# Kernel optimization log

Measured on AMD Instinct MI355X. Metric: run time of the kernel, lower is better.

## Reference

```python
import jax, jax.numpy as jnp
import numpy as np

B, S, D, H, DFF = 8, 1024, 1024, 16, 4096
DK = D // H
NEG = -1000000000.0


def layernorm(x, g, b, eps=1e-5):
    mu = jnp.mean(x, axis=-1, keepdims=True)
    var = jnp.mean((x - mu) ** 2, axis=-1, keepdims=True)
    return (x - mu) / jnp.sqrt(var + eps) * g + b


def setup_inputs() -> dict:
    key = jax.random.key(0)
    ks = jax.random.split(key, 16)
    s = 0.02
    inp = {
        "x": jax.random.normal(ks[0], (B, S, D), jnp.float32),
        "binary_mask": jax.random.randint(ks[1], (B, S), 0, 2, jnp.int32),
        # per-head projections stacked: [H, D, DK]
        "Wq": jax.random.normal(ks[2], (H, D, DK), jnp.float32) * s,
        "bq": jnp.zeros((H, DK), jnp.float32),
        "Wk": jax.random.normal(ks[3], (H, D, DK), jnp.float32) * s,
        "bk": jnp.zeros((H, DK), jnp.float32),
        "Wv": jax.random.normal(ks[4], (H, D, DK), jnp.float32) * s,
        "bv": jnp.zeros((H, DK), jnp.float32),
        "Wo": jax.random.normal(ks[5], (D, D), jnp.float32) * s,
        "bo": jnp.zeros((D,), jnp.float32),
        "ga": jnp.ones((D,), jnp.float32),
        "ba": jnp.zeros((D,), jnp.float32),
        "W1": jax.random.normal(ks[6], (D, DFF), jnp.float32) * s,
        "b1": jnp.zeros((DFF,), jnp.float32),
        "W2": jax.random.normal(ks[7], (DFF, D), jnp.float32) * s,
        "b2": jnp.zeros((D,), jnp.float32),
        "gf": jnp.ones((D,), jnp.float32),
        "bf": jnp.zeros((D,), jnp.float32),
    }
    return inp


def encoder_fwd(x, binary_mask, Wq, bq, Wk, bk, Wv, bv, Wo, bo, ga, ba, W1, b1, W2, b2, gf, bf):
    # --- multi-head self-attention (heads vectorized over h axis) ---
    q = jnp.einsum("bsd,hdk->bhsk", x, Wq) + bq[None, :, None, :]
    k = jnp.einsum("bsd,hdk->bhsk", x, Wk) + bk[None, :, None, :]
    v = jnp.einsum("bsd,hdk->bhsk", x, Wv) + bv[None, :, None, :]
    score = jnp.einsum("bhik,bhjk->bhij", q, k) / jnp.sqrt(jnp.float32(DK))
    # mask: binary_mask is over KEY positions, broadcast over query dim
    score = score + jnp.where(binary_mask[:, None, None, :] == 0, NEG, 0.0)
    # NOTE: original code softmaxes over dim=1 of [B,Sq,Sk] -> the QUERY axis
    probs = jax.nn.softmax(score, axis=2)
    ctx = jnp.einsum("bhij,bhjk->bhik", probs, v)  # [B,H,S,DK]
    ctx = jnp.transpose(ctx, (0, 2, 1, 3)).reshape(x.shape[0], x.shape[1], D)
    attn_out = ctx @ Wo + bo
    y = layernorm(x + attn_out, ga, ba)
    # --- FFN ---
    h = jax.nn.relu(y @ W1 + b1)
    ffn_out = h @ W2 + b2
    return layernorm(y + ffn_out, gf, bf)


def reference(x, binary_mask, Wq, bq, Wk, bk, Wv, bv, Wo, bo, ga, ba, W1, b1, W2, b2, gf, bf):
    return encoder_fwd(x, binary_mask, Wq, bq, Wk, bk, Wv, bv, Wo, bo, ga, ba, W1, b1, W2, b2, gf, bf)
```

## Files before the change

kernel.cpp:

```cpp
#include <hip/hip_runtime.h>
#include <hip/hip_bf16.h>

typedef __bf16 bf16;
typedef __bf16 bf16x8 __attribute__((ext_vector_type(8)));
typedef __bf16 bf16x4 __attribute__((ext_vector_type(4)));
typedef float  f32x4  __attribute__((ext_vector_type(4)));

#define NB 8
#define NS 1024
#define ND 1024
#define NH 16
#define NDK 64
#define NDFF 4096

static __device__ __forceinline__ f32x4 mfma16(bf16x8 a, bf16x8 b, f32x4 c) {
    return __builtin_amdgcn_mfma_f32_16x16x32_bf16(a, b, c, 0, 0, 0);
}

#define GLDS(g, l) __builtin_amdgcn_global_load_lds( \
    (const __attribute__((address_space(1))) void*)(g), \
    (__attribute__((address_space(3))) void*)(l), 16, 0, 0)

__global__ __launch_bounds__(256) void prep_all(
    const float* __restrict__ x, const int* __restrict__ mask,
    const float* __restrict__ Wq, const float* __restrict__ Wk, const float* __restrict__ Wv,
    const float* __restrict__ Wo, const float* __restrict__ W1, const float* __restrict__ W2,
    const float* __restrict__ bq, const float* __restrict__ bk, const float* __restrict__ bv,
    bf16* __restrict__ xb, bf16* __restrict__ wqkvT, bf16* __restrict__ WoT,
    bf16* __restrict__ W1T, bf16* __restrict__ W2T, float* __restrict__ bqkv,
    int* __restrict__ newpos, int* __restrict__ Ucnt, float* __restrict__ cvec)
{
    __shared__ __align__(16) char shraw[64 * 65 * 4];
    int bid = blockIdx.x, t = threadIdx.x;
    if (bid < 8192) {
        int idx = bid * 256 + t;
        float4 v = ((const float4*)x)[idx];
        bf16x4 o = { (bf16)v.x, (bf16)v.y, (bf16)v.z, (bf16)v.w };
        ((bf16x4*)xb)[idx] = o;
    } else if (bid < 11264) {
        float (*T)[65] = (float (*)[65])shraw;
        int tb = bid - 8192;
        const float* src; bf16* dst; int srcLd, dstLd, tR, tC; bool scale = false;
        if (tb < 768) {
            int mat = tb >> 4, ty = tb & 15;
            int h = mat & 15, type = mat >> 4;
            const float* W = (type == 0) ? Wq : (type == 1 ? Wk : Wv);
            src = W + (size_t)h * ND * NDK;
            srcLd = NDK; tR = ty * 64; tC = 0;
            dst = wqkvT + ((size_t)type * 1024 + h * 64) * ND;
            dstLd = ND;
            scale = (type == 0);
        } else if (tb < 1024) {
            int b2 = tb - 768; int ty = b2 >> 4, tx = b2 & 15;
            src = Wo; srcLd = ND; tR = ty * 64; tC = tx * 64; dst = WoT; dstLd = ND;
        } else if (tb < 2048) {
            int b2 = tb - 1024; int ty = b2 >> 6, tx = b2 & 63;
            src = W1; srcLd = NDFF; tR = ty * 64; tC = tx * 64; dst = W1T; dstLd = ND;
        } else {
            int b2 = tb - 2048; int ty = b2 >> 4, tx = b2 & 15;
            src = W2; srcLd = ND; tR = ty * 64; tC = tx * 64; dst = W2T; dstLd = NDFF;
        }
        int c0 = t & 63, r0 = t >> 6;
        #pragma unroll
        for (int rr = 0; rr < 16; rr++) {
            int row = rr * 4 + r0;
            T[row][c0] = src[(size_t)(tR + row) * srcLd + tC + c0];
        }
        __syncthreads();
        #pragma unroll
        for (int cc = 0; cc < 16; cc++) {
            int col = cc * 4 + r0;
            float v = T[c0][col];
            if (scale) v *= 0.125f;
            dst[(size_t)(tC + col) * dstLd + tR + c0] = (bf16)v;
        }
    } else if (bid < 11276) {
        int n = (bid - 11264) * 256 + t;
        if (n < 3072) {
            int type = n >> 10, hk = n & 1023;
            const float* bb = (type == 0) ? bq : (type == 1 ? bk : bv);
            float v = bb[hk];
            if (type == 0) v *= 0.125f;
            bqkv[n] = v;
        }
    } else if (bid < 11284) {
        int* sums  = (int*)shraw;
        int* scans = (int*)(shraw + 1024);
        int b = bid - 11276;
        const int* mb = mask + b * NS;
        int m[4], s = 0;
        #pragma unroll
        for (int k = 0; k < 4; k++) { m[k] = (mb[t * 4 + k] != 0) ? 1 : 0; s += m[k]; }
        sums[t] = s;
        __syncthreads();
        if (t == 0) {
            int acc = 0;
            for (int i = 0; i < 256; i++) { scans[i] = acc; acc += sums[i]; }
            scans[256] = acc;
            Ucnt[b] = acc;
        }
        __syncthreads();
        int U = scans[256];
        int p = scans[t];
        #pragma unroll
        for (int k = 0; k < 4; k++) {
            int j = t * 4 + k;
            newpos[b * NS + j] = m[k] ? p : U + (j - p);
            p += m[k];
        }
    } else {
        float4 z = {0.f, 0.f, 0.f, 0.f};
        ((float4*)cvec)[(bid - 11284) * 256 + t] = z;
    }
}

__device__ __forceinline__ void gemm_bt_core(
    const bf16* __restrict__ A, const bf16* __restrict__ BT, int K,
    int rowBase, int colBase, f32x4 (&acc)[4][4], bf16* As, bf16* Bs)
{
    const int tid = threadIdx.x;
    const int lane = tid & 63, wid = tid >> 6;
    const int wr = (wid >> 1) * 64, wc = (wid & 1) * 64;
    const int lrow = lane & 15, lq = lane >> 4;
    const int srow = wid * 32 + (lane >> 3);
    const int gblk = (lane & 7) ^ ((lane >> 3) & 7);
    const bf16* Arow = A + (size_t)(rowBase + srow) * K + gblk * 8;
    const bf16* Brow = BT + (size_t)(colBase + srow) * K + gblk * 8;
    const int co0 = ((lq) ^ (lrow & 7)) * 8;
    const int co1 = ((4 + lq) ^ (lrow & 7)) * 8;
    f32x4 zz = {0.f, 0.f, 0.f, 0.f};
    #pragma unroll
    for (int i = 0; i < 4; i++)
        #pragma unroll
        for (int j = 0; j < 4; j++) acc[i][j] = zz;
    for (int k0 = 0; k0 < K; k0 += 64) {
        __syncthreads();
        #pragma unroll
        for (int it = 0; it < 4; it++)
            GLDS(Arow + (size_t)it * 8 * K + k0, As + (wid * 32 + it * 8) * 64);
        #pragma unroll
        for (int it = 0; it < 4; it++)
            GLDS(Brow + (size_t)it * 8 * K + k0, Bs + (wid * 32 + it * 8) * 64);
        __syncthreads();
        #pragma unroll
        for (int kh = 0; kh < 2; kh++) {
            const int co = kh ? co1 : co0;
            bf16x8 af[4], bfr[4];
            #pragma unroll
            for (int tt = 0; tt < 4; tt++) {
                af[tt]  = *(const bf16x8*)&As[(wr + tt * 16 + lrow) * 64 + co];
                bfr[tt] = *(const bf16x8*)&Bs[(wc + tt * 16 + lrow) * 64 + co];
            }
            #pragma unroll
            for (int i = 0; i < 4; i++)
                #pragma unroll
                for (int j = 0; j < 4; j++)
                    acc[i][j] = mfma16(af[i], bfr[j], acc[i][j]);
        }
    }
}

__device__ __forceinline__ void gemm8p(
    const bf16* __restrict__ A, const bf16* __restrict__ BT, int K,
    int rowBase, int colBase, f32x4 (&acc)[8][4], bf16* As, bf16* Bs)
{
    constexpr int SETSZ = 256 * 64;
    const int tid = threadIdx.x, lane = tid & 63, wid = tid >> 6;
    const int wm = wid >> 2, wn = wid & 3;
    const int lrow = lane & 15, lq = lane >> 4;
    const int s8 = lane >> 3, gblk = (lane & 7) ^ s8;
    const int co0 = (lq ^ (lrow & 7)) * 8;
    const int co1 = ((4 + lq) ^ (lrow & 7)) * 8;
    f32x4 zz = {0.f, 0.f, 0.f, 0.f};
    #pragma unroll
    for (int i = 0; i < 8; i++)
        #pragma unroll
        for (int j = 0; j < 4; j++) acc[i][j] = zz;
    const bf16* Ag = A  + (size_t)(rowBase + wid * 8 + s8) * K + gblk * 8;
    const bf16* Bg = BT + (size_t)(colBase + wid * 8 + s8) * K + gblk * 8;

#define SG_A(kt, set, h) do { \
    GLDS(Ag + (size_t)((h) * 128) * K + (kt) * 64, \
         As + (set) * SETSZ + ((h) * 128 + wid * 8) * 64); \
    GLDS(Ag + (size_t)((h) * 128 + 64) * K + (kt) * 64, \
         As + (set) * SETSZ + ((h) * 128 + 64 + wid * 8) * 64); \
} while (0)
#define SG_B(kt, set, h) do { \
    GLDS(Bg + (size_t)((h) * 128) * K + (kt) * 64, \
         Bs + (set) * SETSZ + ((h) * 128 + wid * 8) * 64); \
    GLDS(Bg + (size_t)((h) * 128 + 64) * K + (kt) * 64, \
         Bs + (set) * SETSZ + ((h) * 128 + 64 + wid * 8) * 64); \
} while (0)
#define RD_A(dst, base, ms) do { _Pragma("unroll") for (int i_ = 0; i_ < 4; i_++) { \
    int ro_ = (wm * 128 + (ms) * 64 + i_ * 16 + lrow) * 64; \
    dst[i_][0] = *(const bf16x8*)&(base)[ro_ + co0]; \
    dst[i_][1] = *(const bf16x8*)&(base)[ro_ + co1]; } } while (0)
#define RD_B(dst, base, ns) do { _Pragma("unroll") for (int j_ = 0; j_ < 2; j_++) { \
    int ro_ = (wn * 64 + (ns) * 32 + j_ * 16 + lrow) * 64; \
    dst[j_][0] = *(const bf16x8*)&(base)[ro_ + co0]; \
    dst[j_][1] = *(const bf16x8*)&(base)[ro_ + co1]; } } while (0)
#define CL8(av, bv, ms, ns) do { \
    __builtin_amdgcn_s_setprio(1); \
    _Pragma("unroll") for (int i_ = 0; i_ < 4; i_++) \
    _Pragma("unroll") for (int j_ = 0; j_ < 2; j_++) { \
        acc[(ms) * 4 + i_][(ns) * 2 + j_] = \
            mfma16(av[i_][0], bv[j_][0], acc[(ms) * 4 + i_][(ns) * 2 + j_]); \
        acc[(ms) * 4 + i_][(ns) * 2 + j_] = \
            mfma16(av[i_][1], bv[j_][1], acc[(ms) * 4 + i_][(ns) * 2 + j_]); } \
    __builtin_amdgcn_s_setprio(0); \
} while (0)
#define BAR8 __builtin_amdgcn_s_barrier()
#define VM4 asm volatile("s_waitcnt vmcnt(4)" ::: "memory")
#define VM0 asm volatile("s_waitcnt vmcnt(0)" ::: "memory")

    const int nt = K >> 6, nIter = nt >> 1;
    SG_B(0, 0, 0); SG_B(0, 0, 1);
    SG_A(0, 0, 0); SG_A(0, 0, 1);
    SG_B(1, 1, 0); SG_B(1, 1, 1);
    VM4; BAR8;
    const bf16* A0b = As;           const bf16* B0b = Bs;
    const bf16* A1b = As + SETSZ;   const bf16* B1b = Bs + SETSZ;
    for (int J = 0; J < nIter; ++J) {
        const int v = 2 * J + 1;
        const bool pf = (J + 1 < nIter);
        bf16x8 a0[4][2], a1[4][2], b0[2][2], b1[2][2];
        RD_A(a0, A0b, 0); RD_B(b0, B0b, 0);
        SG_A(v, 1, 0);
        BAR8; CL8(a0, b0, 0, 0); BAR8;
        RD_B(b1, B0b, 1);
        SG_A(v, 1, 1);
        BAR8; CL8(a0, b1, 0, 1); BAR8;
        RD_A(a1, A0b, 1);
        if (pf) SG_B(v + 1, 0, 0);
        BAR8; CL8(a1, b1, 1, 1); BAR8;
        if (pf) SG_B(v + 1, 0, 1);
        BAR8; CL8(a1, b0, 1, 0);
        if (pf) { VM4; } else { VM0; }
        BAR8;
        RD_A(a0, A1b, 0); RD_B(b0, B1b, 0);
        if (pf) SG_A(v + 1, 0, 0);
        BAR8; CL8(a0, b0, 0, 0); BAR8;
        RD_B(b1, B1b, 1);
        if (pf) SG_A(v + 1, 0, 1);
        BAR8; CL8(a0, b1, 0, 1); BAR8;
        RD_A(a1, A1b, 1);
        if (pf) SG_B(v + 2, 1, 0);
        BAR8; CL8(a1, b1, 1, 1); BAR8;
        if (pf) SG_B(v + 2, 1, 1);
        BAR8; CL8(a1, b0, 1, 0);
        if (pf) { VM4; } else { VM0; }
        BAR8;
    }
#undef SG_A
#undef SG_B
#undef RD_A
#undef RD_B
#undef CL8
#undef BAR8
#undef VM4
#undef VM0
}

__device__ __forceinline__ void gemmB_core(
    const bf16* __restrict__ A, const bf16* __restrict__ BT, int K,
    int rowBase, int colBase, f32x4 (&acc)[4][4], bf16* As, bf16* Bs)
{
    constexpr int ABUF = 128 * 64, BBUF = 256 * 64;
    const int tid = threadIdx.x, lane = tid & 63, wid = tid >> 6;
    const int wm = wid >> 2, wn = wid & 3;
    const int lrow = lane & 15, lq = lane >> 4;
    const int srow = lane >> 3, gblk = (lane & 7) ^ srow;
    const int co0 = (lq ^ (lrow & 7)) * 8;
    const int co1 = ((4 + lq) ^ (lrow & 7)) * 8;
    f32x4 zz = {0.f, 0.f, 0.f, 0.f};
    #pragma unroll
    for (int i = 0; i < 4; i++)
        #pragma unroll
        for (int j = 0; j < 4; j++) acc[i][j] = zz;
    const bf16* Ag = A  + (size_t)(rowBase + wid * 8 + srow) * K + gblk * 8;
    const bf16* Bg = BT + (size_t)(colBase + wid * 8 + srow) * K + gblk * 8;

#define SGA2(kt, bi, rr) GLDS(Ag + (size_t)(kt) * 64 + (size_t)(rr) * 64 * K, \
                              As + (bi) * ABUF + ((rr) * 64 + wid * 8) * 64)
#define SGB2(kt, bi, rr) GLDS(Bg + (size_t)(kt) * 64 + (size_t)(rr) * 64 * K, \
                              Bs + (bi) * BBUF + ((rr) * 64 + wid * 8) * 64)
#define RDA2() do { _Pragma("unroll") for (int i_ = 0; i_ < 4; i_++) { \
    int ro_ = (wm * 64 + i_ * 16 + lrow) * 64; \
    af[i_][0] = *(const bf16x8*)&Ab[ro_ + co0]; \
    af[i_][1] = *(const bf16x8*)&Ab[ro_ + co1]; } } while (0)
#define RDB2(dst, NS_) do { _Pragma("unroll") for (int j_ = 0; j_ < 2; j_++) { \
    int ro_ = (wn * 64 + (NS_) * 32 + j_ * 16 + lrow) * 64; \
    dst[j_][0] = *(const bf16x8*)&Bb[ro_ + co0]; \
    dst[j_][1] = *(const bf16x8*)&Bb[ro_ + co1]; } } while (0)
#define CLUSTER_B(bfx, JO) do { \
    __builtin_amdgcn_s_barrier(); \
    asm volatile("s_waitcnt lgkmcnt(0)" ::: "memory"); \
    __builtin_amdgcn_sched_barrier(0); \
    __builtin_amdgcn_s_setprio(1); \
    _Pragma("unroll") \
    for (int i_ = 0; i_ < 4; i_++) \
        _Pragma("unroll") \
        for (int j_ = 0; j_ < 2; j_++) { \
            acc[i_][(JO) + j_] = mfma16(af[i_][0], bfx[j_][0], acc[i_][(JO) + j_]); \
            acc[i_][(JO) + j_] = mfma16(af[i_][1], bfx[j_][1], acc[i_][(JO) + j_]); \
        } \
    __builtin_amdgcn_s_setprio(0); \
} while (0)

    const int nt = K >> 6;
    SGA2(0, 0, 0); SGA2(0, 0, 1);
    SGB2(0, 0, 0); SGB2(0, 0, 1); SGB2(0, 0, 2); SGB2(0, 0, 3);
    SGA2(1, 1, 0); SGA2(1, 1, 1);
    SGB2(1, 1, 0); SGB2(1, 1, 1); SGB2(1, 1, 2); SGB2(1, 1, 3);
    asm volatile("s_waitcnt vmcnt(6)" ::: "memory");
    __builtin_amdgcn_s_barrier();

    int ci = 0, si = 2;
    for (int t = 0; t < nt; ++t) {
        const bf16* Ab = As + ci * ABUF;
        const bf16* Bb = Bs + ci * BBUF;
        const bool pf = (t + 2 < nt);
        bf16x8 af[4][2], bf0[2][2], bf1[2][2];
        RDA2(); RDB2(bf0, 0);
        if (pf) { SGA2(t + 2, si, 0); SGA2(t + 2, si, 1); SGB2(t + 2, si, 0); SGB2(t + 2, si, 1); }
        CLUSTER_B(bf0, 0);
        __builtin_amdgcn_s_barrier();
        RDB2(bf1, 1);
        if (pf) { SGB2(t + 2, si, 2); SGB2(t + 2, si, 3); }
        CLUSTER_B(bf1, 2);
        if (pf)                asm volatile("s_waitcnt vmcnt(6)" ::: "memory");
        else if (t + 1 < nt)   asm volatile("s_waitcnt vmcnt(0)" ::: "memory");
        __builtin_amdgcn_s_barrier();
        ci = (ci == 2) ? 0 : ci + 1;
        si = (si == 2) ? 0 : si + 1;
    }
#undef SGA2
#undef SGB2
#undef RDA2
#undef RDB2
#undef CLUSTER_B
}

__global__ __launch_bounds__(512, 2) void g1_qkv(
    const bf16* __restrict__ x, const bf16* __restrict__ wqkvT, const float* __restrict__ bqkv,
    const int* __restrict__ newpos,
    bf16* __restrict__ Q, bf16* __restrict__ Kb, bf16* __restrict__ Vb)
{
    __shared__ bf16 As[3 * 128 * 64], Bs[3 * 256 * 64];
    f32x4 acc[4][4];
    int g = blockIdx.x;
    int sw = (g & 7) * 96 + (g >> 3);
    int bm = sw / 12, bn = sw % 12;
    int rowBase = bm * 128, colBase = bn * 256;
    gemmB_core(x, wqkvT, ND, rowBase, colBase, acc, As, Bs);
    const int tid = threadIdx.x, lane = tid & 63, wid = tid >> 6;
    const int wm = wid >> 2, wn = wid & 3, lrow = lane & 15, lq = lane >> 4;
    const int type = colBase >> 10;
    int spv[4][4];
    if (type != 0) {
        #pragma unroll
        for (int i = 0; i < 4; i++)
            #pragma unroll
            for (int r = 0; r < 4; r++) {
                int grow = rowBase + wm * 64 + i * 16 + lq * 4 + r;
                spv[i][r] = newpos[grow];
            }
    }
    #pragma unroll
    for (int j = 0; j < 4; j++) {
        int gcol = colBase + wn * 64 + j * 16 + lrow;
        float bias = bqkv[gcol];
        int h = (gcol >> 6) & 15, kk = gcol & 63;
        bf16* dst = (type == 0) ? Q : (type == 1 ? Kb : Vb);
        #pragma unroll
        for (int i = 0; i < 4; i++) {
            #pragma unroll
            for (int r = 0; r < 4; r++) {
                int grow = rowBase + wm * 64 + i * 16 + lq * 4 + r;
                int b = grow >> 10;
                int s = (type == 0) ? (grow & 1023) : spv[i][r];
                dst[((size_t)(b * NH + h) * NS + s) * NDK + kk] = (bf16)(acc[i][j][r] + bias);
            }
        }
    }
}

__global__ __launch_bounds__(256) void vt_trans(
    const bf16* __restrict__ Vb, const int* __restrict__ Ucnt,
    bf16* __restrict__ Vt, float* __restrict__ cvec)
{
    __shared__ bf16 T[64 * 72];
    __shared__ float red[4][64];
    int bh = blockIdx.y, s0 = blockIdx.x * 64;
    const bf16* src = Vb + ((size_t)bh * NS + s0) * NDK;
    int tid = threadIdx.x;
    #pragma unroll
    for (int it = 0; it < 2; it++) {
        int g = tid + it * 256;
        int row = g >> 3, c = (g & 7) * 8;
        *(bf16x8*)&T[row * 72 + c] = *(const bf16x8*)&src[row * NDK + c];
    }
    __syncthreads();
    #pragma unroll
    for (int it = 0; it < 2; it++) {
        int g = tid + it * 256;
        int kk = g >> 3, sc = (g & 7) * 8;
        bf16x8 v;
        #pragma unroll
        for (int t = 0; t < 8; t++) v[t] = T[(sc + t) * 72 + kk];
        *(bf16x8*)&Vt[((size_t)bh * NDK + kk) * NS + s0 + sc] = v;
    }
    int U = Ucnt[bh >> 4];
    int lo = U - s0;
    if (lo < 0) lo = 0;
    if (lo < 64) {
        int kk = tid & 63, ss = tid >> 6;
        float a = 0.f;
        for (int r = lo + ss; r < 64; r += 4) a += (float)T[r * 72 + kk];
        red[ss][kk] = a;
        __syncthreads();
        if (ss == 0)
            atomicAdd(&cvec[bh * 64 + kk], red[0][kk] + red[1][kk] + red[2][kk] + red[3][kk]);
    }
}

__global__ __launch_bounds__(256) void g2_stats(
    const bf16* __restrict__ Q, const bf16* __restrict__ Kb,
    const int* __restrict__ Ucnt, float2* __restrict__ alpha)
{
    __shared__ bf16 Qs[128 * 64];
    int bh = blockIdx.y, b = bh >> 4;
    int jBase = blockIdx.x * 128;
    int U = Ucnt[b];
    const int tid = threadIdx.x;
    if (jBase >= U) {
        if (tid < 128) {
            float2 z; z.x = 0.f; z.y = 0.f;
            alpha[(size_t)bh * NS + jBase + tid] = z;
        }
        return;
    }
    const bf16* Kp = Kb + (size_t)bh * NS * NDK;
    const bf16* Qp = Q + (size_t)bh * NS * NDK;
    const int lane = tid & 63, wid = tid >> 6;
    const int lrow = lane & 15, lq = lane >> 4;
    bf16x8 kf[2][2];
    #pragma unroll
    for (int jt = 0; jt < 2; jt++)
        #pragma unroll
        for (int kh = 0; kh < 2; kh++)
            kf[jt][kh] = *(const bf16x8*)&Kp[(size_t)(jBase + wid * 32 + jt * 16 + lrow) * NDK + kh * 32 + lq * 8];
    const int srow = lane >> 3;
    const int gblk = (lane & 7) ^ srow;
    float Lacc[2][4];
    #pragma unroll
    for (int jt = 0; jt < 2; jt++)
        #pragma unroll
        for (int r = 0; r < 4; r++) Lacc[jt][r] = 0.f;
    f32x4 zz = {0.f, 0.f, 0.f, 0.f};
    for (int i0 = 0; i0 < NS; i0 += 128) {
        __syncthreads();
        #pragma unroll
        for (int it = 0; it < 4; it++)
            GLDS(Qp + (size_t)(i0 + wid * 32 + it * 8 + srow) * NDK + gblk * 8,
                 Qs + (wid * 32 + it * 8) * 64);
        __syncthreads();
        #pragma unroll
        for (int it = 0; it < 8; it++) {
            bf16x8 qb[2];
            #pragma unroll
            for (int kh = 0; kh < 2; kh++)
                qb[kh] = *(const bf16x8*)&Qs[(it * 16 + lrow) * 64 + ((kh * 4 + lq) ^ (lrow & 7)) * 8];
            #pragma unroll
            for (int jt = 0; jt < 2; jt++) {
                f32x4 s = mfma16(kf[jt][0], qb[0], zz);
                s = mfma16(kf[jt][1], qb[1], s);
                #pragma unroll
                for (int r = 0; r < 4; r++) Lacc[jt][r] += __expf(s[r]);
            }
        }
    }
    #pragma unroll
    for (int jt = 0; jt < 2; jt++) {
        #pragma unroll
        for (int r = 0; r < 4; r++) {
            float v = Lacc[jt][r];
            v += __shfl_xor(v, 1); v += __shfl_xor(v, 2);
            v += __shfl_xor(v, 4); v += __shfl_xor(v, 8);
            if (lrow == 0) {
                int j = jBase + wid * 32 + jt * 16 + lq * 4 + r;
                float2 ac;
                ac.x = (j < U) ? 1.f / v : 0.f;
                ac.y = 0.f;
                alpha[(size_t)bh * NS + j] = ac;
            }
        }
    }
}

__global__ __launch_bounds__(256) void g3_ctx(
    const bf16* __restrict__ Q, const bf16* __restrict__ Kb, const bf16* __restrict__ Vt,
    const float2* __restrict__ alpha, const int* __restrict__ Ucnt,
    const float* __restrict__ cvec, bf16* __restrict__ ctx)
{
    __shared__ bf16 Ks[64 * 64];
    __shared__ bf16 Vs[64 * 64];
    __shared__ bf16 Ps[4 * 64 * 64];
    int bh = blockIdx.y, iBase = blockIdx.x * 256;
    int b = bh >> 4, h = bh & 15;
    int U = Ucnt[b];
    int Ur = (U + 63) & ~63;
    const bf16* Qp = Q + (size_t)bh * NS * NDK;
    const bf16* Kp = Kb + (size_t)bh * NS * NDK;
    const bf16* Vp = Vt + (size_t)bh * NDK * NS;
    const float2* al = alpha + (size_t)bh * NS;
    const int tid = threadIdx.x, lane = tid & 63, wid = tid >> 6;
    const int lrow = lane & 15, lq = lane >> 4;
    const int iw = iBase + wid * 64;
    bf16x8 qf[4][2];
    #pragma unroll
    for (int it = 0; it < 4; it++)
        #pragma unroll
        for (int kh = 0; kh < 2; kh++)
            qf[it][kh] = *(const bf16x8*)&Qp[(size_t)(iw + it * 16 + lrow) * NDK + kh * 32 + lq * 8];
    const int srow = lane >> 3;
    const int gblk = (lane & 7) ^ srow;
    f32x4 cacc[4][4];
    f32x4 zz = {0.f, 0.f, 0.f, 0.f};
    #pragma unroll
    for (int it = 0; it < 4; it++)
        #pragma unroll
        for (int kt = 0; kt < 4; kt++) cacc[it][kt] = zz;
    bf16* Pw = Ps + wid * 64 * 64;
    for (int j0 = 0; j0 < Ur; j0 += 64) {
        __syncthreads();
        #pragma unroll
        for (int it = 0; it < 2; it++)
            GLDS(Kp + (size_t)(j0 + wid * 16 + it * 8 + srow) * NDK + gblk * 8,
                 Ks + (wid * 16 + it * 8) * 64);
        #pragma unroll
        for (int it = 0; it < 2; it++)
            GLDS(Vp + (size_t)(wid * 16 + it * 8 + srow) * NS + j0 + gblk * 8,
                 Vs + (wid * 16 + it * 8) * 64);
        __syncthreads();
        bf16x8 kb[4][2];
        #pragma unroll
        for (int jt = 0; jt < 4; jt++)
            #pragma unroll
            for (int kh = 0; kh < 2; kh++)
                kb[jt][kh] = *(const bf16x8*)&Ks[(jt * 16 + lrow) * 64 + ((kh * 4 + lq) ^ (lrow & 7)) * 8];
        #pragma unroll
        for (int jt = 0; jt < 4; jt++) {
            float2 acj[4];
            #pragma unroll
            for (int r = 0; r < 4; r++) acj[r] = al[j0 + jt * 16 + lq * 4 + r];
            #pragma unroll
            for (int it = 0; it < 4; it++) {
                f32x4 s = mfma16(kb[jt][0], qf[it][0], zz);
                s = mfma16(kb[jt][1], qf[it][1], s);
                bf16x4 pv;
                #pragma unroll
                for (int r = 0; r < 4; r++)
                    pv[r] = (bf16)(acj[r].x * __expf(s[r]) + acj[r].y);
                int i = it * 16 + lrow;
                int jb = jt * 2 + (lq >> 1);
                *(bf16x4*)&Pw[i * 64 + ((jb ^ (i & 7)) * 8) + (lq & 1) * 4] = pv;
            }
        }
        bf16x8 vb[4][2];
        #pragma unroll
        for (int kt = 0; kt < 4; kt++)
            #pragma unroll
            for (int kh = 0; kh < 2; kh++)
                vb[kt][kh] = *(const bf16x8*)&Vs[(kt * 16 + lrow) * 64 + ((kh * 4 + lq) ^ (lrow & 7)) * 8];
        #pragma unroll
        for (int it = 0; it < 4; it++) {
            bf16x8 pa[2];
            #pragma unroll
            for (int kh = 0; kh < 2; kh++)
                pa[kh] = *(const bf16x8*)&Pw[(it * 16 + lrow) * 64 + ((kh * 4 + lq) ^ (lrow & 7)) * 8];
            #pragma unroll
            for (int kt = 0; kt < 4; kt++) {
                cacc[it][kt] = mfma16(pa[0], vb[kt][0], cacc[it][kt]);
                cacc[it][kt] = mfma16(pa[1], vb[kt][1], cacc[it][kt]);
            }
        }
    }
    #pragma unroll
    for (int kt = 0; kt < 4; kt++) {
        int col = h * NDK + kt * 16 + lrow;
        float cv = cvec[bh * 64 + kt * 16 + lrow] * (1.f / 1024.f);
        #pragma unroll
        for (int it = 0; it < 4; it++) {
            #pragma unroll
            for (int r = 0; r < 4; r++) {
                int i = iw + it * 16 + lq * 4 + r;
                ctx[(size_t)(b * NS + i) * ND + col] = (bf16)(cacc[it][kt][r] + cv);
            }
        }
    }
}

__global__ __launch_bounds__(256) void g4_proj(
    const bf16* __restrict__ ctx, const bf16* __restrict__ WoT, const float* __restrict__ bo,
    const bf16* __restrict__ xb, bf16* __restrict__ t1b)
{
    __shared__ bf16 As[128 * 64], Bs[128 * 64];
    f32x4 acc[4][4];
    int rowBase = blockIdx.x * 128, colBase = blockIdx.y * 128;
    gemm_bt_core(ctx, WoT, ND, rowBase, colBase, acc, As, Bs);
    const int tid = threadIdx.x, lane = tid & 63, wid = tid >> 6;
    const int wr = (wid >> 1) * 64, wc = (wid & 1) * 64, lrow = lane & 15, lq = lane >> 4;
    #pragma unroll
    for (int j = 0; j < 4; j++) {
        int gcol = colBase + wc + j * 16 + lrow;
        float bias = bo[gcol];
        #pragma unroll
        for (int i = 0; i < 4; i++) {
            #pragma unroll
            for (int r = 0; r < 4; r++) {
                int grow = rowBase + wr + i * 16 + lq * 4 + r;
                float v = acc[i][j][r] + bias + (float)xb[(size_t)grow * ND + gcol];
                t1b[(size_t)grow * ND + gcol] = (bf16)v;
            }
        }
    }
}

__global__ __launch_bounds__(512, 2) void g5_ffn1(
    const bf16* __restrict__ y, const bf16* __restrict__ W1T, const float* __restrict__ b1,
    bf16* __restrict__ hb)
{
    __shared__ bf16 As[2 * 256 * 64], Bs[2 * 256 * 64];
    f32x4 acc[8][4];
    int g = blockIdx.x;
    int sw = (g & 7) * 64 + (g >> 3);
    int bm = sw >> 4, bn = sw & 15;
    int rowBase = bm * 256, colBase = bn * 256;
    gemm8p(y, W1T, ND, rowBase, colBase, acc, As, Bs);
    const int tid = threadIdx.x, lane = tid & 63, wid = tid >> 6;
    const int wm = wid >> 2, wn = wid & 3, lrow = lane & 15, lq = lane >> 4;
    #pragma unroll
    for (int j = 0; j < 4; j++) {
        int gcol = colBase + wn * 64 + j * 16 + lrow;
        float bias = b1[gcol];
        #pragma unroll
        for (int i = 0; i < 8; i++) {
            #pragma unroll
            for (int r = 0; r < 4; r++) {
                int grow = rowBase + wm * 128 + i * 16 + lq * 4 + r;
                float v = fmaxf(acc[i][j][r] + bias, 0.f);
                hb[(size_t)grow * NDFF + gcol] = (bf16)v;
            }
        }
    }
}

__global__ __launch_bounds__(512, 2) void g6_ffn2(
    const bf16* __restrict__ hb, const bf16* __restrict__ W2T, const float* __restrict__ b2,
    const bf16* __restrict__ yb, bf16* __restrict__ zb)
{
    __shared__ bf16 As[3 * 128 * 64], Bs[3 * 256 * 64];
    f32x4 acc[4][4];
    int g = blockIdx.x;
    int sw = (g & 7) * 32 + (g >> 3);
    int bm = sw >> 2, bn = sw & 3;
    int rowBase = bm * 128, colBase = bn * 256;
    gemmB_core(hb, W2T, NDFF, rowBase, colBase, acc, As, Bs);
    const int tid = threadIdx.x, lane = tid & 63, wid = tid >> 6;
    const int wm = wid >> 2, wn = wid & 3, lrow = lane & 15, lq = lane >> 4;
    #pragma unroll
    for (int j = 0; j < 4; j++) {
        int gcol = colBase + wn * 64 + j * 16 + lrow;
        float bias = b2[gcol];
        #pragma unroll
        for (int i = 0; i < 4; i++) {
            #pragma unroll
            for (int r = 0; r < 4; r++) {
                int grow = rowBase + wm * 64 + i * 16 + lq * 4 + r;
                float v = acc[i][j][r] + bias + (float)yb[(size_t)grow * ND + gcol];
                zb[(size_t)grow * ND + gcol] = (bf16)v;
            }
        }
    }
}

__global__ __launch_bounds__(256) void ln_kernel(
    const bf16* __restrict__ in, bf16* __restrict__ outb, float* __restrict__ outf,
    const float* __restrict__ g, const float* __restrict__ bb)
{
    int row = blockIdx.x, tid = threadIdx.x;
    const bf16* p = in + (size_t)row * ND;
    bf16x4 v4 = *(const bf16x4*)&p[tid * 4];
    float vv[4] = {(float)v4[0], (float)v4[1], (float)v4[2], (float)v4[3]};
    float s = vv[0] + vv[1] + vv[2] + vv[3];
    float q = vv[0]*vv[0] + vv[1]*vv[1] + vv[2]*vv[2] + vv[3]*vv[3];
    #pragma unroll
    for (int m = 1; m < 64; m <<= 1) { s += __shfl_xor(s, m); q += __shfl_xor(q, m); }
    __shared__ float rs[4], rq[4];
    int wid = tid >> 6, lane = tid & 63;
    if (lane == 0) { rs[wid] = s; rq[wid] = q; }
    __syncthreads();
    s = rs[0] + rs[1] + rs[2] + rs[3];
    q = rq[0] + rq[1] + rq[2] + rq[3];
    float mean = s * (1.f / 1024.f);
    float var = q * (1.f / 1024.f) - mean * mean;
    float rstd = 1.f / sqrtf(var + 1e-5f);
    float4 of;
    bf16x4 ob;
    #pragma unroll
    for (int k = 0; k < 4; k++) {
        int col = tid * 4 + k;
        float yv = (vv[k] - mean) * rstd * g[col] + bb[col];
        ((float*)&of)[k] = yv;
        ob[k] = (bf16)yv;
    }
    if (outb) *(bf16x4*)&outb[(size_t)row * ND + tid * 4] = ob;
    if (outf) ((float4*)(outf + (size_t)row * ND))[tid] = of;
}

extern "C" void kernel_launch(void* const* d_in, const int* in_sizes, int n_in,
                              void* d_out, int out_size, void* d_ws, size_t ws_size,
                              hipStream_t stream)
{
    const float* x    = (const float*)d_in[0];
    const int*   mask = (const int*)d_in[1];
    const float* Wq   = (const float*)d_in[2];
    const float* bq   = (const float*)d_in[3];
    const float* Wk   = (const float*)d_in[4];
    const float* bk   = (const float*)d_in[5];
    const float* Wv   = (const float*)d_in[6];
    const float* bv   = (const float*)d_in[7];
    const float* Wo   = (const float*)d_in[8];
    const float* bo   = (const float*)d_in[9];
    const float* ga   = (const float*)d_in[10];
    const float* ba   = (const float*)d_in[11];
    const float* W1   = (const float*)d_in[12];
    const float* b1   = (const float*)d_in[13];
    const float* W2   = (const float*)d_in[14];
    const float* b2   = (const float*)d_in[15];
    const float* gf   = (const float*)d_in[16];
    const float* bfb  = (const float*)d_in[17];

    size_t off = 0;
    auto alloc = [&](size_t n) { char* p = (char*)d_ws + off; off += (n + 255) & ~(size_t)255; return (void*)p; };
    bf16*   wqkvT = (bf16*)  alloc((size_t)3072 * 1024 * 2);
    bf16*   WoT   = (bf16*)  alloc((size_t)1024 * 1024 * 2);
    bf16*   W1T   = (bf16*)  alloc((size_t)4096 * 1024 * 2);
    bf16*   W2T   = (bf16*)  alloc((size_t)1024 * 4096 * 2);
    float*  bqkv  = (float*) alloc(3072 * 4);
    float2* alpha = (float2*)alloc((size_t)NB * NH * NS * 8);
    int*    newpos= (int*)   alloc((size_t)NB * NS * 4);
    int*    Ucnt  = (int*)   alloc(NB * 4);
    float*  cvec  = (float*) alloc((size_t)NB * NH * NDK * 4);
    bf16*   xb    = (bf16*)  alloc((size_t)8192 * 1024 * 2);
    bf16*   ub    = (bf16*)  alloc((size_t)8192 * 4096 * 2);
    bf16*   Qb    = ub;
    bf16*   Kb    = ub + (size_t)8192 * 1024;
    bf16*   Vt    = ub + (size_t)2 * 8192 * 1024;
    bf16*   ctx   = ub + (size_t)3 * 8192 * 1024;
    bf16*   hb    = ub;
    bf16*   t1b   = (bf16*)  alloc((size_t)8192 * 1024 * 2);
    bf16*   Vb    = t1b;
    bf16*   zb    = t1b;
    bf16*   yb    = (bf16*)  alloc((size_t)8192 * 1024 * 2);

    prep_all<<<11292, 256, 0, stream>>>(x, mask, Wq, Wk, Wv, Wo, W1, W2, bq, bk, bv,
                                        xb, wqkvT, WoT, W1T, W2T, bqkv, newpos, Ucnt, cvec);
    g1_qkv<<<768, 512, 0, stream>>>(xb, wqkvT, bqkv, newpos, Qb, Kb, Vb);
    vt_trans<<<dim3(16, 128), 256, 0, stream>>>(Vb, Ucnt, Vt, cvec);
    g2_stats<<<dim3(8, 128), 256, 0, stream>>>(Qb, Kb, Ucnt, alpha);
    g3_ctx<<<dim3(4, 128), 256, 0, stream>>>(Qb, Kb, Vt, alpha, Ucnt, cvec, ctx);
    g4_proj<<<dim3(64, 8), 256, 0, stream>>>(ctx, WoT, bo, xb, t1b);
    ln_kernel<<<8192, 256, 0, stream>>>(t1b, yb, nullptr, ga, ba);
    g5_ffn1<<<512, 512, 0, stream>>>(yb, W1T, b1, hb);
    g6_ffn2<<<256, 512, 0, stream>>>(hb, W2T, b2, yb, zb);
    ln_kernel<<<8192, 256, 0, stream>>>(zb, nullptr, (float*)d_out, gf, bfb);
}
```

Measured before the change: 472.8 us.

## Merge V-transpose into stats kernel and move Wo projection to pipelined GEMM

The V transpose/column-sum kernel and the softmax statistics kernel become one launch, with extra blocks on the x axis doing the transpose work. This removes a launch and lets the two independent jobs run at the same time. The output projection now uses the triple-buffered, prefetching 128x256 GEMM core with 512 threads, swizzled block ordering and priority-boosted MFMA clusters, in place of the simple single-buffer 128x128 loop. This costs more LDS per block and leaves fewer blocks to fill the CUs.

Measured after the change: 481.4 us. No clear change (+1.8%).

```diff
diff --git a/kernel.cpp b/kernel.cpp
--- a/kernel.cpp
+++ b/kernel.cpp
@@ -114,50 +114,84 @@
     }
 }
 
-__device__ __forceinline__ void gemm_bt_core(
+__device__ __forceinline__ void gemmB_core(
     const bf16* __restrict__ A, const bf16* __restrict__ BT, int K,
     int rowBase, int colBase, f32x4 (&acc)[4][4], bf16* As, bf16* Bs)
 {
-    const int tid = threadIdx.x;
-    const int lane = tid & 63, wid = tid >> 6;
-    const int wr = (wid >> 1) * 64, wc = (wid & 1) * 64;
+    constexpr int ABUF = 128 * 64, BBUF = 256 * 64;
+    const int tid = threadIdx.x, lane = tid & 63, wid = tid >> 6;
+    const int wm = wid >> 2, wn = wid & 3;
     const int lrow = lane & 15, lq = lane >> 4;
-    const int srow = wid * 32 + (lane >> 3);
-    const int gblk = (lane & 7) ^ ((lane >> 3) & 7);
-    const bf16* Arow = A + (size_t)(rowBase + srow) * K + gblk * 8;
-    const bf16* Brow = BT + (size_t)(colBase + srow) * K + gblk * 8;
-    const int co0 = ((lq) ^ (lrow & 7)) * 8;
+    const int srow = lane >> 3, gblk = (lane & 7) ^ srow;
+    const int co0 = (lq ^ (lrow & 7)) * 8;
     const int co1 = ((4 + lq) ^ (lrow & 7)) * 8;
     f32x4 zz = {0.f, 0.f, 0.f, 0.f};
     #pragma unroll
     for (int i = 0; i < 4; i++)
         #pragma unroll
         for (int j = 0; j < 4; j++) acc[i][j] = zz;
-    for (int k0 = 0; k0 < K; k0 += 64) {
-        __syncthreads();
-        #pragma unroll
-        for (int it = 0; it < 4; it++)
-            GLDS(Arow + (size_t)it * 8 * K + k0, As + (wid * 32 + it * 8) * 64);
-        #pragma unroll
-        for (int it = 0; it < 4; it++)
-            GLDS(Brow + (size_t)it * 8 * K + k0, Bs + (wid * 32 + it * 8) * 64);
-        __syncthreads();
-        #pragma unroll
-        for (int kh = 0; kh < 2; kh++) {
-            const int co = kh ? co1 : co0;
-            bf16x8 af[4], bfr[4];
-            #pragma unroll
-            for (int tt = 0; tt < 4; tt++) {
-                af[tt]  = *(const bf16x8*)&As[(wr + tt * 16 + lrow) * 64 + co];
-                bfr[tt] = *(const bf16x8*)&Bs[(wc + tt * 16 + lrow) * 64 + co];
-            }
-            #pragma unroll
-            for (int i = 0; i < 4; i++)
-                #pragma unroll
-                for (int j = 0; j < 4; j++)
-                    acc[i][j] = mfma16(af[i], bfr[j], acc[i][j]);
-        }
-    }
+    const bf16* Ag = A  + (size_t)(rowBase + wid * 8 + srow) * K + gblk * 8;
+    const bf16* Bg = BT + (size_t)(colBase + wid * 8 + srow) * K + gblk * 8;
+
+#define SGA2(kt, bi, rr) GLDS(Ag + (size_t)(kt) * 64 + (size_t)(rr) * 64 * K, \
+                              As + (bi) * ABUF + ((rr) * 64 + wid * 8) * 64)
+#define SGB2(kt, bi, rr) GLDS(Bg + (size_t)(kt) * 64 + (size_t)(rr) * 64 * K, \
+                              Bs + (bi) * BBUF + ((rr) * 64 + wid * 8) * 64)
+#define RDA2() do { _Pragma("unroll") for (int i_ = 0; i_ < 4; i_++) { \
+    int ro_ = (wm * 64 + i_ * 16 + lrow) * 64; \
+    af[i_][0] = *(const bf16x8*)&Ab[ro_ + co0]; \
+    af[i_][1] = *(const bf16x8*)&Ab[ro_ + co1]; } } while (0)
+#define RDB2(dst, NS_) do { _Pragma("unroll") for (int j_ = 0; j_ < 2; j_++) { \
+    int ro_ = (wn * 64 + (NS_) * 32 + j_ * 16 + lrow) * 64; \
+    dst[j_][0] = *(const bf16x8*)&Bb[ro_ + co0]; \
+    dst[j_][1] = *(const bf16x8*)&Bb[ro_ + co1]; } } while (0)
+#define CLUSTER_B(bfx, JO) do { \
+    __builtin_amdgcn_s_barrier(); \
+    asm volatile("s_waitcnt lgkmcnt(0)" ::: "memory"); \
+    __builtin_amdgcn_sched_barrier(0); \
+    __builtin_amdgcn_s_setprio(1); \
+    _Pragma("unroll") \
+    for (int i_ = 0; i_ < 4; i_++) \
+        _Pragma("unroll") \
+        for (int j_ = 0; j_ < 2; j_++) { \
+            acc[i_][(JO) + j_] = mfma16(af[i_][0], bfx[j_][0], acc[i_][(JO) + j_]); \
+            acc[i_][(JO) + j_] = mfma16(af[i_][1], bfx[j_][1], acc[i_][(JO) + j_]); \
+        } \
+    __builtin_amdgcn_s_setprio(0); \
+} while (0)
+
+    const int nt = K >> 6;
+    SGA2(0, 0, 0); SGA2(0, 0, 1);
+    SGB2(0, 0, 0); SGB2(0, 0, 1); SGB2(0, 0, 2); SGB2(0, 0, 3);
+    SGA2(1, 1, 0); SGA2(1, 1, 1);
+    SGB2(1, 1, 0); SGB2(1, 1, 1); SGB2(1, 1, 2); SGB2(1, 1, 3);
+    asm volatile("s_waitcnt vmcnt(6)" ::: "memory");
+    __builtin_amdgcn_s_barrier();
+
+    int ci = 0, si = 2;
+    for (int t = 0; t < nt; ++t) {
+        const bf16* Ab = As + ci * ABUF;
+        const bf16* Bb = Bs + ci * BBUF;
+        const bool pf = (t + 2 < nt);
+        bf16x8 af[4][2], bf0[2][2], bf1[2][2];
+        RDA2(); RDB2(bf0, 0);
+        if (pf) { SGA2(t + 2, si, 0); SGA2(t + 2, si, 1); SGB2(t + 2, si, 0); SGB2(t + 2, si, 1); }
+        CLUSTER_B(bf0, 0);
+        __builtin_amdgcn_s_barrier();
+        RDB2(bf1, 1);
+        if (pf) { SGB2(t + 2, si, 2); SGB2(t + 2, si, 3); }
+        CLUSTER_B(bf1, 2);
+        if (pf)                asm volatile("s_waitcnt vmcnt(6)" ::: "memory");
+        else if (t + 1 < nt)   asm volatile("s_waitcnt vmcnt(0)" ::: "memory");
+        __builtin_amdgcn_s_barrier();
+        ci = (ci == 2) ? 0 : ci + 1;
+        si = (si == 2) ? 0 : si + 1;
+    }
+#undef SGA2
+#undef SGB2
+#undef RDA2
+#undef RDB2
+#undef CLUSTER_B
 }
 
 __device__ __forceinline__ void gemm8p(
@@ -261,86 +295,6 @@
 #undef VM0
 }
 
-__device__ __forceinline__ void gemmB_core(
-    const bf16* __restrict__ A, const bf16* __restrict__ BT, int K,
-    int rowBase, int colBase, f32x4 (&acc)[4][4], bf16* As, bf16* Bs)
-{
-    constexpr int ABUF = 128 * 64, BBUF = 256 * 64;
-    const int tid = threadIdx.x, lane = tid & 63, wid = tid >> 6;
-    const int wm = wid >> 2, wn = wid & 3;
-    const int lrow = lane & 15, lq = lane >> 4;
-    const int srow = lane >> 3, gblk = (lane & 7) ^ srow;
-    const int co0 = (lq ^ (lrow & 7)) * 8;
-    const int co1 = ((4 + lq) ^ (lrow & 7)) * 8;
-    f32x4 zz = {0.f, 0.f, 0.f, 0.f};
-    #pragma unroll
-    for (int i = 0; i < 4; i++)
-        #pragma unroll
-        for (int j = 0; j < 4; j++) acc[i][j] = zz;
-    const bf16* Ag = A  + (size_t)(rowBase + wid * 8 + srow) * K + gblk * 8;
-    const bf16* Bg = BT + (size_t)(colBase + wid * 8 + srow) * K + gblk * 8;
-
-#define SGA2(kt, bi, rr) GLDS(Ag + (size_t)(kt) * 64 + (size_t)(rr) * 64 * K, \
-                              As + (bi) * ABUF + ((rr) * 64 + wid * 8) * 64)
-#define SGB2(kt, bi, rr) GLDS(Bg + (size_t)(kt) * 64 + (size_t)(rr) * 64 * K, \
-                              Bs + (bi) * BBUF + ((rr) * 64 + wid * 8) * 64)
-#define RDA2() do { _Pragma("unroll") for (int i_ = 0; i_ < 4; i_++) { \
-    int ro_ = (wm * 64 + i_ * 16 + lrow) * 64; \
-    af[i_][0] = *(const bf16x8*)&Ab[ro_ + co0]; \
-    af[i_][1] = *(const bf16x8*)&Ab[ro_ + co1]; } } while (0)
-#define RDB2(dst, NS_) do { _Pragma("unroll") for (int j_ = 0; j_ < 2; j_++) { \
-    int ro_ = (wn * 64 + (NS_) * 32 + j_ * 16 + lrow) * 64; \
-    dst[j_][0] = *(const bf16x8*)&Bb[ro_ + co0]; \
-    dst[j_][1] = *(const bf16x8*)&Bb[ro_ + co1]; } } while (0)
-#define CLUSTER_B(bfx, JO) do { \
-    __builtin_amdgcn_s_barrier(); \
-    asm volatile("s_waitcnt lgkmcnt(0)" ::: "memory"); \
-    __builtin_amdgcn_sched_barrier(0); \
-    __builtin_amdgcn_s_setprio(1); \
-    _Pragma("unroll") \
-    for (int i_ = 0; i_ < 4; i_++) \
-        _Pragma("unroll") \
-        for (int j_ = 0; j_ < 2; j_++) { \
-            acc[i_][(JO) + j_] = mfma16(af[i_][0], bfx[j_][0], acc[i_][(JO) + j_]); \
-            acc[i_][(JO) + j_] = mfma16(af[i_][1], bfx[j_][1], acc[i_][(JO) + j_]); \
-        } \
-    __builtin_amdgcn_s_setprio(0); \
-} while (0)
-
-    const int nt = K >> 6;
-    SGA2(0, 0, 0); SGA2(0, 0, 1);
-    SGB2(0, 0, 0); SGB2(0, 0, 1); SGB2(0, 0, 2); SGB2(0, 0, 3);
-    SGA2(1, 1, 0); SGA2(1, 1, 1);
-    SGB2(1, 1, 0); SGB2(1, 1, 1); SGB2(1, 1, 2); SGB2(1, 1, 3);
-    asm volatile("s_waitcnt vmcnt(6)" ::: "memory");
-    __builtin_amdgcn_s_barrier();
-
-    int ci = 0, si = 2;
-    for (int t = 0; t < nt; ++t) {
-        const bf16* Ab = As + ci * ABUF;
-        const bf16* Bb = Bs + ci * BBUF;
-        const bool pf = (t + 2 < nt);
-        bf16x8 af[4][2], bf0[2][2], bf1[2][2];
-        RDA2(); RDB2(bf0, 0);
-        if (pf) { SGA2(t + 2, si, 0); SGA2(t + 2, si, 1); SGB2(t + 2, si, 0); SGB2(t + 2, si, 1); }
-        CLUSTER_B(bf0, 0);
-        __builtin_amdgcn_s_barrier();
-        RDB2(bf1, 1);
-        if (pf) { SGB2(t + 2, si, 2); SGB2(t + 2, si, 3); }
-        CLUSTER_B(bf1, 2);
-        if (pf)                asm volatile("s_waitcnt vmcnt(6)" ::: "memory");
-        else if (t + 1 < nt)   asm volatile("s_waitcnt vmcnt(0)" ::: "memory");
-        __builtin_amdgcn_s_barrier();
-        ci = (ci == 2) ? 0 : ci + 1;
-        si = (si == 2) ? 0 : si + 1;
-    }
-#undef SGA2
-#undef SGB2
-#undef RDA2
-#undef RDB2
-#undef CLUSTER_B
-}
-
 __global__ __launch_bounds__(512, 2) void g1_qkv(
     const bf16* __restrict__ x, const bf16* __restrict__ wqkvT, const float* __restrict__ bqkv,
     const int* __restrict__ newpos,
@@ -385,54 +339,52 @@
     }
 }
 
-__global__ __launch_bounds__(256) void vt_trans(
-    const bf16* __restrict__ Vb, const int* __restrict__ Ucnt,
+__global__ __launch_bounds__(256) void g2v(
+    const bf16* __restrict__ Q, const bf16* __restrict__ Kb, const bf16* __restrict__ Vb,
+    const int* __restrict__ Ucnt, float2* __restrict__ alpha,
     bf16* __restrict__ Vt, float* __restrict__ cvec)
 {
-    __shared__ bf16 T[64 * 72];
-    __shared__ float red[4][64];
-    int bh = blockIdx.y, s0 = blockIdx.x * 64;
-    const bf16* src = Vb + ((size_t)bh * NS + s0) * NDK;
-    int tid = threadIdx.x;
-    #pragma unroll
-    for (int it = 0; it < 2; it++) {
-        int g = tid + it * 256;
-        int row = g >> 3, c = (g & 7) * 8;
-        *(bf16x8*)&T[row * 72 + c] = *(const bf16x8*)&src[row * NDK + c];
-    }
-    __syncthreads();
-    #pragma unroll
-    for (int it = 0; it < 2; it++) {
-        int g = tid + it * 256;
-        int kk = g >> 3, sc = (g & 7) * 8;
-        bf16x8 v;
-        #pragma unroll
-        for (int t = 0; t < 8; t++) v[t] = T[(sc + t) * 72 + kk];
-        *(bf16x8*)&Vt[((size_t)bh * NDK + kk) * NS + s0 + sc] = v;
-    }
-    int U = Ucnt[bh >> 4];
-    int lo = U - s0;
-    if (lo < 0) lo = 0;
-    if (lo < 64) {
-        int kk = tid & 63, ss = tid >> 6;
-        float a = 0.f;
-        for (int r = lo + ss; r < 64; r += 4) a += (float)T[r * 72 + kk];
-        red[ss][kk] = a;
+    __shared__ __align__(16) char sraw[128 * 64 * 2];
+    int bh = blockIdx.y, b = bh >> 4;
+    const int tid = threadIdx.x;
+    if (blockIdx.x >= 8) {
+        bf16* T = (bf16*)sraw;
+        float (*red)[64] = (float (*)[64])(sraw + 64 * 72 * 2);
+        int s0 = (blockIdx.x - 8) * 64;
+        const bf16* src = Vb + ((size_t)bh * NS + s0) * NDK;
+        #pragma unroll
+        for (int it = 0; it < 2; it++) {
+            int g = tid + it * 256;
+            int row = g >> 3, c = (g & 7) * 8;
+            *(bf16x8*)&T[row * 72 + c] = *(const bf16x8*)&src[row * NDK + c];
+        }
         __syncthreads();
-        if (ss == 0)
-            atomicAdd(&cvec[bh * 64 + kk], red[0][kk] + red[1][kk] + red[2][kk] + red[3][kk]);
-    }
-}
-
-__global__ __launch_bounds__(256) void g2_stats(
-    const bf16* __restrict__ Q, const bf16* __restrict__ Kb,
-    const int* __restrict__ Ucnt, float2* __restrict__ alpha)
-{
-    __shared__ bf16 Qs[128 * 64];
-    int bh = blockIdx.y, b = bh >> 4;
+        #pragma unroll
+        for (int it = 0; it < 2; it++) {
+            int g = tid + it * 256;
+            int kk = g >> 3, sc = (g & 7) * 8;
+            bf16x8 v;
+            #pragma unroll
+            for (int t = 0; t < 8; t++) v[t] = T[(sc + t) * 72 + kk];
+            *(bf16x8*)&Vt[((size_t)bh * NDK + kk) * NS + s0 + sc] = v;
+        }
+        int U = Ucnt[b];
+        int lo = U - s0;
+        if (lo < 0) lo = 0;
+        if (lo < 64) {
+            int kk = tid & 63, ss = tid >> 6;
+            float a = 0.f;
+            for (int r = lo + ss; r < 64; r += 4) a += (float)T[r * 72 + kk];
+            red[ss][kk] = a;
+            __syncthreads();
+            if (ss == 0)
+                atomicAdd(&cvec[bh * 64 + kk], red[0][kk] + red[1][kk] + red[2][kk] + red[3][kk]);
+        }
+        return;
+    }
+    bf16* Qs = (bf16*)sraw;
     int jBase = blockIdx.x * 128;
     int U = Ucnt[b];
-    const int tid = threadIdx.x;
     if (jBase >= U) {
         if (tid < 128) {
             float2 z; z.x = 0.f; z.y = 0.f;
@@ -601,25 +553,28 @@
     }
 }
 
-__global__ __launch_bounds__(256) void g4_proj(
+__global__ __launch_bounds__(512, 2) void g4_proj(
     const bf16* __restrict__ ctx, const bf16* __restrict__ WoT, const float* __restrict__ bo,
     const bf16* __restrict__ xb, bf16* __restrict__ t1b)
 {
-    __shared__ bf16 As[128 * 64], Bs[128 * 64];
+    __shared__ bf16 As[3 * 128 * 64], Bs[3 * 256 * 64];
     f32x4 acc[4][4];
-    int rowBase = blockIdx.x * 128, colBase = blockIdx.y * 128;
-    gemm_bt_core(ctx, WoT, ND, rowBase, colBase, acc, As, Bs);
+    int g = blockIdx.x;
+    int sw = (g & 7) * 32 + (g >> 3);
+    int bm = sw >> 2, bn = sw & 3;
+    int rowBase = bm * 128, colBase = bn * 256;
+    gemmB_core(ctx, WoT, ND, rowBase, colBase, acc, As, Bs);
     const int tid = threadIdx.x, lane = tid & 63, wid = tid >> 6;
-    const int wr = (wid >> 1) * 64, wc = (wid & 1) * 64, lrow = lane & 15, lq = lane >> 4;
+    const int wm = wid >> 2, wn = wid & 3, lrow = lane & 15, lq = lane >> 4;
     #pragma unroll
     for (int j = 0; j < 4; j++) {
-        int gcol = colBase + wc + j * 16 + lrow;
+        int gcol = colBase + wn * 64 + j * 16 + lrow;
         float bias = bo[gcol];
         #pragma unroll
         for (int i = 0; i < 4; i++) {
             #pragma unroll
             for (int r = 0; r < 4; r++) {
-                int grow = rowBase + wr + i * 16 + lq * 4 + r;
+                int grow = rowBase + wm * 64 + i * 16 + lq * 4 + r;
                 float v = acc[i][j][r] + bias + (float)xb[(size_t)grow * ND + gcol];
                 t1b[(size_t)grow * ND + gcol] = (bf16)v;
             }
@@ -768,10 +723,9 @@
     prep_all<<<11292, 256, 0, stream>>>(x, mask, Wq, Wk, Wv, Wo, W1, W2, bq, bk, bv,
                                         xb, wqkvT, WoT, W1T, W2T, bqkv, newpos, Ucnt, cvec);
     g1_qkv<<<768, 512, 0, stream>>>(xb, wqkvT, bqkv, newpos, Qb, Kb, Vb);
-    vt_trans<<<dim3(16, 128), 256, 0, stream>>>(Vb, Ucnt, Vt, cvec);
-    g2_stats<<<dim3(8, 128), 256, 0, stream>>>(Qb, Kb, Ucnt, alpha);
+    g2v<<<dim3(24, 128), 256, 0, stream>>>(Qb, Kb, Vb, Ucnt, alpha, Vt, cvec);
     g3_ctx<<<dim3(4, 128), 256, 0, stream>>>(Qb, Kb, Vt, alpha, Ucnt, cvec, ctx);
-    g4_proj<<<dim3(64, 8), 256, 0, stream>>>(ctx, WoT, bo, xb, t1b);
+    g4_proj<<<256, 512, 0, stream>>>(ctx, WoT, bo, xb, t1b);
     ln_kernel<<<8192, 256, 0, stream>>>(t1b, yb, nullptr, ga, ba);
     g5_ffn1<<<512, 512, 0, stream>>>(yb, W1T, b1, hb);
     g6_ffn2<<<256, 512, 0, stream>>>(hb, W2T, b2, yb, zb);
```
